# Performance work log

Hardware: AMD Instinct MI355X
Metric: run time of the kernel (lower is better)

## Reference

```python
import jax, jax.numpy as jnp
import numpy as np

NUM_CLASS = 31
B = 4096
F_IN = 2048
F_BOT = 256


def setup_inputs() -> dict:
    key = jax.random.key(0)
    ks = jax.random.split(key, 6)
    return {
        "source": jax.random.normal(ks[0], (B, F_IN), dtype=jnp.float32),
        "target": jax.random.normal(ks[1], (B, F_IN), dtype=jnp.float32),
        "W_b": jax.random.normal(ks[2], (F_IN, F_BOT), dtype=jnp.float32) * (1.0 / np.sqrt(F_IN)),
        "b_b": jnp.zeros((F_BOT,), dtype=jnp.float32),
        "W_c": jax.random.normal(ks[3], (F_BOT, NUM_CLASS), dtype=jnp.float32) * (1.0 / np.sqrt(F_BOT)),
        "b_c": jnp.zeros((NUM_CLASS,), dtype=jnp.float32),
        "source_label": jax.random.randint(ks[4], (B,), 0, NUM_CLASS, dtype=jnp.int64),
    }


def _conf_margin(logits, labels):
    # get_confidence_output_margin: softmax confidence margin vs best wrong class
    conf = jax.nn.softmax(logits, axis=-1)
    mask = jax.nn.one_hot(labels, NUM_CLASS, dtype=conf.dtype)
    targets_conf = jnp.sum(conf * mask, axis=1)
    max_excl_conf = jnp.max(conf * (1.0 - mask), axis=1)
    return targets_conf - max_excl_conf


def _pairwise_sqdist(s, t):
    # ||x_p - x_q||^2 computed as a single GEMM + broadcast (replaces python double loop)
    s2 = jnp.sum(s * s, axis=1)  # [Bs]
    t2 = jnp.sum(t * t, axis=1)  # [Bt]
    d2 = s2[:, None] + t2[None, :] - 2.0 * (s @ t.T)
    return jnp.maximum(d2, 0.0)


def reference(source, target, W_b, b_b, W_c, b_c, source_label):
    # bottleneck: Linear + ReLU (shared weights for both domains)
    src = jax.nn.relu(source @ W_b + b_b)  # [B, 256]
    tar = jax.nn.relu(target @ W_b + b_b)  # [B, 256]

    src_clf = src @ W_c + b_c  # [B, 31]
    tar_clf = tar @ W_c + b_c  # [B, 31]

    # cross entropy on source
    logp = jax.nn.log_softmax(src_clf, axis=-1)
    clf_loss = -jnp.mean(jnp.take_along_axis(logp, source_label[:, None], axis=1))

    src_margin = _conf_margin(src_clf, source_label)
    tar_margin = _conf_margin(tar_clf, jnp.argmax(tar_clf, axis=1))

    # no_grad diagnostics: MMD + Gaussian kernel means (amplitude=1, sigma in {1,5})
    delta = jnp.mean(src, axis=0) - jnp.mean(tar, axis=0)
    curr_mmd = jax.lax.stop_gradient(delta @ delta)
    d2 = _pairwise_sqdist(src, tar)  # [B, B]
    curr_gk1 = jax.lax.stop_gradient(jnp.mean(jnp.exp(-0.5 * d2)))
    curr_gk5 = jax.lax.stop_gradient(jnp.mean(jnp.exp(-d2 / 50.0)))

    return jnp.concatenate([
        jnp.stack([clf_loss, curr_mmd, curr_gk1, curr_gk5]),
        src_margin,
        tar_margin,
    ])  # [4 + 2B]
```

## Files before the change

### kernel.cpp

```cpp
#include <hip/hip_runtime.h>
#include <hip/hip_bf16.h>
#include <stdint.h>

#define DI __device__ __forceinline__

typedef float f32x4 __attribute__((ext_vector_type(4)));
typedef short bf16x8 __attribute__((ext_vector_type(8)));

DI uint16_t f2bf(float f) {
    union { float f; uint32_t u; } v; v.f = f;
    uint32_t r = v.u + 0x7FFF + ((v.u >> 16) & 1);
    return (uint16_t)(r >> 16);
}
DI float bf2f(uint16_t h) {
    union { uint32_t u; float f; } v; v.u = ((uint32_t)h) << 16;
    return v.f;
}
DI uint32_t pk_bf16(float x, float y) {
    __hip_bfloat162 h = __float22bfloat162_rn(make_float2(x, y));
    union { __hip_bfloat162 h; uint32_t u; } v; v.h = h; return v.u;
}
DI void gl_lds16(const void* g, void* l) {
    __builtin_amdgcn_global_load_lds(
        (__attribute__((address_space(1))) void*)(uintptr_t)g,
        (__attribute__((address_space(3))) void*)(uintptr_t)l,
        16, 0, 0);
}

__global__ void k_prep(const float* __restrict__ Wb, uint16_t* __restrict__ WbT,
                       const float* __restrict__ Wc, uint16_t* __restrict__ WcT) {
    if (blockIdx.x == 512) {
        int tid = threadIdx.x;
        for (int idx = tid; idx < 32 * 256; idx += 256) {
            int n = idx >> 8, k = idx & 255;
            WcT[idx] = (n < 31) ? f2bf(Wc[k * 31 + n]) : (uint16_t)0;
        }
        return;
    }
    __shared__ float t[32][33];
    int kb = blockIdx.x & 63, nb = blockIdx.x >> 6;
    int tx = threadIdx.x & 31, ty0 = (threadIdx.x >> 5) * 4;
    for (int i = 0; i < 4; ++i)
        t[ty0 + i][tx] = Wb[(kb * 32 + ty0 + i) * 256 + nb * 32 + tx];
    __syncthreads();
    for (int i = 0; i < 4; ++i)
        WbT[(nb * 32 + ty0 + i) * 2048 + kb * 32 + tx] = f2bf(t[tx][ty0 + i]);
}

__launch_bounds__(256, 4)
__global__ void k_bottleneck(const float* __restrict__ src, const float* __restrict__ tgt,
                             const uint16_t* __restrict__ WbT, const float* __restrict__ bbias,
                             uint16_t* __restrict__ Y) {
    __shared__ __align__(16) uint8_t lds[24576];
    int tid = threadIdx.x, lane = tid & 63, w = tid >> 6;
    int bm = blockIdx.x >> 2, bn = blockIdx.x & 3;
    int rowbase = bm * 32, n0 = bn * 64;
    const float* Xr = (rowbase < 4096) ? src + (size_t)rowbase * 2048
                                       : tgt + (size_t)(rowbase - 4096) * 2048;
    int rl = lane & 15, kq = lane >> 4;

    int as = tid >> 6;
    const float* Ag = Xr + (size_t)((as & 1) * 16 + rl) * 2048 + (as >> 1) * 32 + kq * 8;
    uint8_t* Aw0 = lds + tid * 16;
    uint8_t* Aw1 = lds + 4096 + tid * 16;

    const uint16_t* Bg[4];
    uint8_t* Bl[4];
    for (int i = 0; i < 4; ++i) {
        int sb = w * 4 + i, kb = sb >> 2, wseg = sb & 3;
        Bg[i] = WbT + (size_t)(n0 + wseg * 16 + rl) * 2048 + kb * 32 + kq * 8;
        Bl[i] = lds + 8192 + sb * 1024;
    }

    f32x4 acc[2] = {};
    for (int t = 0; t < 16; ++t) {
        if (t) __syncthreads();
        int k0 = t * 128;
        for (int i = 0; i < 4; ++i) gl_lds16(Bg[i] + k0, Bl[i]);
        float4 x0 = *(const float4*)(Ag + k0);
        float4 x1 = *(const float4*)(Ag + k0 + 4);
        float4 x2 = *(const float4*)(Ag + k0 + 64);
        float4 x3 = *(const float4*)(Ag + k0 + 68);
        uint4 u0, u1;
        u0.x = pk_bf16(x0.x, x0.y); u0.y = pk_bf16(x0.z, x0.w);
        u0.z = pk_bf16(x1.x, x1.y); u0.w = pk_bf16(x1.z, x1.w);
        u1.x = pk_bf16(x2.x, x2.y); u1.y = pk_bf16(x2.z, x2.w);
        u1.z = pk_bf16(x3.x, x3.y); u1.w = pk_bf16(x3.z, x3.w);
        *(uint4*)Aw0 = u0;
        *(uint4*)Aw1 = u1;
        __syncthreads();
#pragma unroll
        for (int kb = 0; kb < 4; ++kb) {
            bf16x8 a0 = *(const bf16x8*)(lds + kb * 2048 + lane * 16);
            bf16x8 a1 = *(const bf16x8*)(lds + kb * 2048 + 1024 + lane * 16);
            bf16x8 b  = *(const bf16x8*)(lds + 8192 + kb * 4096 + w * 1024 + lane * 16);
            acc[0] = __builtin_amdgcn_mfma_f32_16x16x32_bf16(a0, b, acc[0], 0, 0, 0);
            acc[1] = __builtin_amdgcn_mfma_f32_16x16x32_bf16(a1, b, acc[1], 0, 0, 0);
        }
    }
    int col = n0 + w * 16 + rl;
    float bias = bbias[col];
    for (int mi = 0; mi < 2; ++mi)
        for (int j = 0; j < 4; ++j) {
            int row = rowbase + mi * 16 + kq * 4 + j;
            float v = fmaxf(acc[mi][j] + bias, 0.f);
            Y[(size_t)row * 256 + col] = f2bf(v);
        }
}

__global__ void k_stats(const uint16_t* __restrict__ Y, float* __restrict__ s2t2,
                        float* __restrict__ part) {
    __shared__ float sred[4][256];
    int tid = threadIdx.x, cg = tid & 63, rs = tid >> 6;
    int r0 = blockIdx.x * 16;
    float a0 = 0.f, a1 = 0.f, a2 = 0.f, a3 = 0.f;
    for (int it = 0; it < 4; ++it) {
        int row = r0 + it * 4 + rs;
        ushort4 v = *(const ushort4*)(Y + (size_t)row * 256 + cg * 4);
        float f0 = bf2f(v.x), f1 = bf2f(v.y), f2 = bf2f(v.z), f3 = bf2f(v.w);
        a0 += f0; a1 += f1; a2 += f2; a3 += f3;
        float s = f0 * f0 + f1 * f1 + f2 * f2 + f3 * f3;
        for (int m = 1; m < 64; m <<= 1) s += __shfl_xor(s, m);
        if (cg == 0) s2t2[row] = s;
    }
    sred[rs][cg * 4 + 0] = a0; sred[rs][cg * 4 + 1] = a1;
    sred[rs][cg * 4 + 2] = a2; sred[rs][cg * 4 + 3] = a3;
    __syncthreads();
    if (rs == 0)
        for (int i = 0; i < 4; ++i) {
            int col = cg * 4 + i;
            part[blockIdx.x * 256 + col] =
                sred[0][col] + sred[1][col] + sred[2][col] + sred[3][col];
        }
}

__launch_bounds__(64)
__global__ void k_classifier(const uint16_t* __restrict__ Y, const uint16_t* __restrict__ WcT,
                             const float* __restrict__ bc, const int* __restrict__ labels,
                             float* __restrict__ out_margin, float* __restrict__ ce_part) {
    int lane = threadIdx.x;
    int r0 = blockIdx.x * 16;
    bool is_src = (r0 < 4096);
    int rl = lane & 15, kq = lane >> 4;
    const uint16_t* Ap = Y + (size_t)(r0 + rl) * 256 + kq * 8;
    const uint16_t* Bp = WcT + (size_t)rl * 256 + kq * 8;
    f32x4 acc[2] = {};
#pragma unroll
    for (int kb = 0; kb < 8; ++kb) {
        bf16x8 a  = *(const bf16x8*)(Ap + kb * 32);
        bf16x8 b0 = *(const bf16x8*)(Bp + kb * 32);
        bf16x8 b1 = *(const bf16x8*)(Bp + 16 * 256 + kb * 32);
        acc[0] = __builtin_amdgcn_mfma_f32_16x16x32_bf16(a, b0, acc[0], 0, 0, 0);
        acc[1] = __builtin_amdgcn_mfma_f32_16x16x32_bf16(a, b1, acc[1], 0, 0, 0);
    }
    int c0 = rl, c1 = 16 + rl;
    float bc0 = bc[c0];
    float bc1 = (c1 < 31) ? bc[c1] : 0.f;
    float ce_local = 0.f;
    for (int j = 0; j < 4; ++j) {
        int row = r0 + kq * 4 + j;
        float v0 = acc[0][j] + bc0;
        float v1 = (c1 < 31) ? (acc[1][j] + bc1) : -1e30f;
        float mx = fmaxf(v0, v1);
        for (int m = 1; m < 16; m <<= 1) mx = fmaxf(mx, __shfl_xor(mx, m, 16));
        float e0 = __expf(v0 - mx);
        float e1 = (c1 < 31) ? __expf(v1 - mx) : 0.f;
        float ssum = e0 + e1;
        for (int m = 1; m < 16; m <<= 1) ssum += __shfl_xor(ssum, m, 16);
        float inv = 1.f / ssum;
        float conf0 = e0 * inv, conf1 = e1 * inv;
        int lab;
        if (is_src) {
            lab = labels[row];
        } else {
            float bv; int bi;
            if (v0 >= v1) { bv = v0; bi = c0; } else { bv = v1; bi = c1; }
            for (int m = 1; m < 16; m <<= 1) {
                float ov = __shfl_xor(bv, m, 16);
                int oi = __shfl_xor(bi, m, 16);
                if (ov > bv || (ov == bv && oi < bi)) { bv = ov; bi = oi; }
            }
            lab = bi;
        }
        float tc = (c0 == lab ? conf0 : 0.f) + (c1 == lab ? conf1 : 0.f);
        for (int m = 1; m < 16; m <<= 1) tc += __shfl_xor(tc, m, 16);
        float ex = fmaxf(c0 == lab ? -1.f : conf0,
                         (c1 == lab || c1 >= 31) ? -1.f : conf1);
        for (int m = 1; m < 16; m <<= 1) ex = fmaxf(ex, __shfl_xor(ex, m, 16));
        if (c0 == 0) out_margin[row] = tc - ex;
        if (is_src) {
            float vl = (c0 == lab) ? v0 : ((c1 == lab) ? v1 : -1e30f);
            for (int m = 1; m < 16; m <<= 1) vl = fmaxf(vl, __shfl_xor(vl, m, 16));
            if (c0 == 0) ce_local += -(vl - mx - __logf(ssum));
        }
    }
    ce_local += __shfl_xor(ce_local, 16);
    ce_local += __shfl_xor(ce_local, 32);
    if (lane == 0) ce_part[blockIdx.x] = is_src ? ce_local : 0.f;
}

__launch_bounds__(256)
__global__ void k_pairwise(const uint16_t* __restrict__ Y, const float* __restrict__ s2t2,
                           float* __restrict__ gk_part) {
    __shared__ __align__(16) uint8_t lds[32768];
    int tid = threadIdx.x, lane = tid & 63, w = tid >> 6;
    int m0 = blockIdx.x * 128, n0 = blockIdx.y * 128;
    int cc = (lane >> 4) ^ (lane & 3) ^ ((lane >> 2) & 3);
    int wm = (w & 1) * 64, wn = (w >> 1) * 64;
    f32x4 acc[4][4] = {};
    for (int h = 0; h < 4; ++h) {
        if (h) __syncthreads();
        int k0 = h * 64;
        for (int i = 0; i < 4; ++i) {
            int s = w * 4 + i;
            int kb = s >> 3, r0 = (s & 7) * 16;
            int r = r0 + (lane >> 2), p = lane & 3;
            int c = p ^ (r & 3) ^ ((r >> 2) & 3);
            gl_lds16(Y + (size_t)(m0 + r) * 256 + k0 + kb * 32 + c * 8, lds + s * 1024);
            gl_lds16(Y + (size_t)(4096 + n0 + r) * 256 + k0 + kb * 32 + c * 8,
                     lds + 16384 + s * 1024);
        }
        __syncthreads();
        for (int kb = 0; kb < 2; ++kb) {
            bf16x8 a[4], b[4];
            for (int mi = 0; mi < 4; ++mi) {
                int r = wm + mi * 16 + (lane & 15);
                a[mi] = *(const bf16x8*)(lds + kb * 8192 + r * 64 + cc * 16);
            }
            for (int nf = 0; nf < 4; ++nf) {
                int rn = wn + nf * 16 + (lane & 15);
                b[nf] = *(const bf16x8*)(lds + 16384 + kb * 8192 + rn * 64 + cc * 16);
            }
            for (int mi = 0; mi < 4; ++mi)
                for (int nf = 0; nf < 4; ++nf)
                    acc[mi][nf] = __builtin_amdgcn_mfma_f32_16x16x32_bf16(
                        a[mi], b[nf], acc[mi][nf], 0, 0, 0);
        }
    }
    float t2v[4];
    for (int nf = 0; nf < 4; ++nf)
        t2v[nf] = s2t2[4096 + n0 + wn + nf * 16 + (lane & 15)];
    float g1 = 0.f, g5 = 0.f;
    for (int mi = 0; mi < 4; ++mi) {
        int rbase = m0 + wm + mi * 16 + (lane >> 4) * 4;
        float s2v[4];
        for (int j = 0; j < 4; ++j) s2v[j] = s2t2[rbase + j];
        for (int nf = 0; nf < 4; ++nf)
            for (int j = 0; j < 4; ++j) {
                float d2 = s2v[j] + t2v[nf] - 2.f * acc[mi][nf][j];
                d2 = fmaxf(d2, 0.f);
                g1 += __expf(-0.5f * d2);
                g5 += __expf(-0.02f * d2);
            }
    }
    for (int m = 1; m < 64; m <<= 1) { g1 += __shfl_xor(g1, m); g5 += __shfl_xor(g5, m); }
    __syncthreads();
    float* red = (float*)lds;
    if (lane == 0) { red[w * 2] = g1; red[w * 2 + 1] = g5; }
    __syncthreads();
    if (tid == 0) {
        int bid = blockIdx.y * 32 + blockIdx.x;
        gk_part[bid * 2]     = red[0] + red[2] + red[4] + red[6];
        gk_part[bid * 2 + 1] = red[1] + red[3] + red[5] + red[7];
    }
}

__global__ void k_finalize(const float* __restrict__ colsum_part,
                           const float* __restrict__ gk_part,
                           const float* __restrict__ ce_part, float* __restrict__ d_out) {
    __shared__ float red[4][4];
    int tid = threadIdx.x, lane = tid & 63, w = tid >> 6;
    float cs = 0.f, ct = 0.f;
    for (int b = 0; b < 256; ++b)   cs += colsum_part[b * 256 + tid];
    for (int b = 256; b < 512; ++b) ct += colsum_part[b * 256 + tid];
    float delta = (cs - ct) * (1.f / 4096.f);
    float sq = delta * delta;
    float g1 = 0.f, g5 = 0.f;
    for (int i = 0; i < 4; ++i) {
        int p = tid * 4 + i;
        g1 += gk_part[p * 2];
        g5 += gk_part[p * 2 + 1];
    }
    float ce = ce_part[tid] + ce_part[tid + 256];
    for (int m = 1; m < 64; m <<= 1) {
        sq += __shfl_xor(sq, m);
        g1 += __shfl_xor(g1, m);
        g5 += __shfl_xor(g5, m);
        ce += __shfl_xor(ce, m);
    }
    if (lane == 0) { red[w][0] = sq; red[w][1] = g1; red[w][2] = g5; red[w][3] = ce; }
    __syncthreads();
    if (tid == 0) {
        d_out[0] = (red[0][3] + red[1][3] + red[2][3] + red[3][3]) * (1.f / 4096.f);
        d_out[1] = red[0][0] + red[1][0] + red[2][0] + red[3][0];
        d_out[2] = (red[0][1] + red[1][1] + red[2][1] + red[3][1]) * 5.9604644775390625e-08f;
        d_out[3] = (red[0][2] + red[1][2] + red[2][2] + red[3][2]) * 5.9604644775390625e-08f;
    }
}

extern "C" void kernel_launch(void* const* d_in, const int* in_sizes, int n_in,
                              void* d_out, int out_size, void* d_ws, size_t ws_size,
                              hipStream_t stream) {
    const float* source = (const float*)d_in[0];
    const float* target = (const float*)d_in[1];
    const float* Wb     = (const float*)d_in[2];
    const float* bb     = (const float*)d_in[3];
    const float* Wc     = (const float*)d_in[4];
    const float* bc     = (const float*)d_in[5];
    const int*   labels = (const int*)d_in[6];
    float* out = (float*)d_out;
    uint8_t* ws = (uint8_t*)d_ws;

    uint16_t* Y    = (uint16_t*)(ws);
    uint16_t* WbT  = (uint16_t*)(ws + 4194304);
    uint16_t* WcT  = (uint16_t*)(ws + 5242880);
    float*    s2t2 = (float*)(ws + 5259264);
    float* colsum_part = (float*)(ws + 4194304);
    float* gk_part     = (float*)(ws + 4194304 + 524288);
    float* ce_part     = (float*)(ws + 4194304 + 532480);

    k_prep<<<513, 256, 0, stream>>>(Wb, WbT, Wc, WcT);
    k_bottleneck<<<1024, 256, 0, stream>>>(source, target, WbT, bb, Y);
    k_stats<<<512, 256, 0, stream>>>(Y, s2t2, colsum_part);
    k_classifier<<<512, 64, 0, stream>>>(Y, WcT, bc, labels, out + 4, ce_part);
    k_pairwise<<<dim3(32, 32), 256, 0, stream>>>(Y, s2t2, gk_part);
    k_finalize<<<1, 256, 0, stream>>>(colsum_part, gk_part, ce_part, out);
}
```

Before: 203.3 us.

## Double-buffer bottleneck GEMM with register-resident A and wider N tiles

```diff
diff --git a/kernel.cpp b/kernel.cpp
--- a/kernel.cpp
+++ b/kernel.cpp
@@ -47,64 +47,98 @@
         WbT[(nb * 32 + ty0 + i) * 2048 + kb * 32 + tx] = f2bf(t[tx][ty0 + i]);
 }
 
-__launch_bounds__(256, 4)
+__launch_bounds__(256, 2)
 __global__ void k_bottleneck(const float* __restrict__ src, const float* __restrict__ tgt,
                              const uint16_t* __restrict__ WbT, const float* __restrict__ bbias,
                              uint16_t* __restrict__ Y) {
-    __shared__ __align__(16) uint8_t lds[24576];
+    __shared__ __align__(16) uint8_t lds[32768];
     int tid = threadIdx.x, lane = tid & 63, w = tid >> 6;
-    int bm = blockIdx.x >> 2, bn = blockIdx.x & 3;
-    int rowbase = bm * 32, n0 = bn * 64;
+    int bm = blockIdx.x >> 1, bn = blockIdx.x & 1;
+    int rowbase = bm * 32, n0 = bn * 128;
     const float* Xr = (rowbase < 4096) ? src + (size_t)rowbase * 2048
                                        : tgt + (size_t)(rowbase - 4096) * 2048;
     int rl = lane & 15, kq = lane >> 4;
 
-    int as = tid >> 6;
-    const float* Ag = Xr + (size_t)((as & 1) * 16 + rl) * 2048 + (as >> 1) * 32 + kq * 8;
-    uint8_t* Aw0 = lds + tid * 16;
-    uint8_t* Aw1 = lds + 4096 + tid * 16;
+    const float* Ab = Xr + (size_t)rl * 2048 + kq * 8;
 
     const uint16_t* Bg[4];
     uint8_t* Bl[4];
     for (int i = 0; i < 4; ++i) {
-        int sb = w * 4 + i, kb = sb >> 2, wseg = sb & 3;
-        Bg[i] = WbT + (size_t)(n0 + wseg * 16 + rl) * 2048 + kb * 32 + kq * 8;
-        Bl[i] = lds + 8192 + sb * 1024;
-    }
-
-    f32x4 acc[2] = {};
-    for (int t = 0; t < 16; ++t) {
-        if (t) __syncthreads();
-        int k0 = t * 128;
-        for (int i = 0; i < 4; ++i) gl_lds16(Bg[i] + k0, Bl[i]);
-        float4 x0 = *(const float4*)(Ag + k0);
-        float4 x1 = *(const float4*)(Ag + k0 + 4);
-        float4 x2 = *(const float4*)(Ag + k0 + 64);
-        float4 x3 = *(const float4*)(Ag + k0 + 68);
-        uint4 u0, u1;
-        u0.x = pk_bf16(x0.x, x0.y); u0.y = pk_bf16(x0.z, x0.w);
-        u0.z = pk_bf16(x1.x, x1.y); u0.w = pk_bf16(x1.z, x1.w);
-        u1.x = pk_bf16(x2.x, x2.y); u1.y = pk_bf16(x2.z, x2.w);
-        u1.z = pk_bf16(x3.x, x3.y); u1.w = pk_bf16(x3.z, x3.w);
-        *(uint4*)Aw0 = u0;
-        *(uint4*)Aw1 = u1;
+        int s = w * 4 + i, kb = s >> 3, nf = s & 7;
+        Bg[i] = WbT + (size_t)(n0 + nf * 16 + rl) * 2048 + kb * 32 + kq * 8;
+        Bl[i] = lds + s * 1024;
+    }
+
+    f32x4 acc[2][2] = {};
+    float4 a0[2][2][2], a1[2][2][2];
+
+    for (int i = 0; i < 4; ++i) gl_lds16(Bg[i], Bl[i]);
+#pragma unroll
+    for (int mi = 0; mi < 2; ++mi)
+#pragma unroll
+        for (int kb = 0; kb < 2; ++kb) {
+            const float* p = Ab + (size_t)mi * 16 * 2048 + kb * 32;
+            a0[mi][kb][0] = *(const float4*)(p);
+            a0[mi][kb][1] = *(const float4*)(p + 4);
+        }
+    __syncthreads();
+
+#pragma unroll
+    for (int t = 0; t < 32; ++t) {
+        const int cur = t & 1;
+        if (t < 31) {
+            int k0n = (t + 1) * 64;
+#pragma unroll
+            for (int mi = 0; mi < 2; ++mi)
+#pragma unroll
+                for (int kb = 0; kb < 2; ++kb) {
+                    const float* p = Ab + (size_t)mi * 16 * 2048 + kb * 32 + k0n;
+                    if (cur == 0) {
+                        a1[mi][kb][0] = *(const float4*)(p);
+                        a1[mi][kb][1] = *(const float4*)(p + 4);
+                    } else {
+                        a0[mi][kb][0] = *(const float4*)(p);
+                        a0[mi][kb][1] = *(const float4*)(p + 4);
+                    }
+                }
+            for (int i = 0; i < 4; ++i)
+                gl_lds16(Bg[i] + k0n, Bl[i] + (cur ^ 1) * 16384);
+        }
+        union { uint4 u; bf16x8 v; } af[2][2];
+#pragma unroll
+        for (int mi = 0; mi < 2; ++mi)
+#pragma unroll
+            for (int kb = 0; kb < 2; ++kb) {
+                float4 x0 = (cur == 0) ? a0[mi][kb][0] : a1[mi][kb][0];
+                float4 x1 = (cur == 0) ? a0[mi][kb][1] : a1[mi][kb][1];
+                af[mi][kb].u.x = pk_bf16(x0.x, x0.y);
+                af[mi][kb].u.y = pk_bf16(x0.z, x0.w);
+                af[mi][kb].u.z = pk_bf16(x1.x, x1.y);
+                af[mi][kb].u.w = pk_bf16(x1.z, x1.w);
+            }
+#pragma unroll
+        for (int kb = 0; kb < 2; ++kb)
+#pragma unroll
+            for (int nfl = 0; nfl < 2; ++nfl) {
+                bf16x8 b = *(const bf16x8*)(lds + cur * 16384 +
+                                            (kb * 8 + w * 2 + nfl) * 1024 + lane * 16);
+                acc[0][nfl] = __builtin_amdgcn_mfma_f32_16x16x32_bf16(
+                    af[0][kb].v, b, acc[0][nfl], 0, 0, 0);
+                acc[1][nfl] = __builtin_amdgcn_mfma_f32_16x16x32_bf16(
+                    af[1][kb].v, b, acc[1][nfl], 0, 0, 0);
+            }
         __syncthreads();
-#pragma unroll
-        for (int kb = 0; kb < 4; ++kb) {
-            bf16x8 a0 = *(const bf16x8*)(lds + kb * 2048 + lane * 16);
-            bf16x8 a1 = *(const bf16x8*)(lds + kb * 2048 + 1024 + lane * 16);
-            bf16x8 b  = *(const bf16x8*)(lds + 8192 + kb * 4096 + w * 1024 + lane * 16);
-            acc[0] = __builtin_amdgcn_mfma_f32_16x16x32_bf16(a0, b, acc[0], 0, 0, 0);
-            acc[1] = __builtin_amdgcn_mfma_f32_16x16x32_bf16(a1, b, acc[1], 0, 0, 0);
-        }
-    }
-    int col = n0 + w * 16 + rl;
-    float bias = bbias[col];
+    }
+
     for (int mi = 0; mi < 2; ++mi)
-        for (int j = 0; j < 4; ++j) {
-            int row = rowbase + mi * 16 + kq * 4 + j;
-            float v = fmaxf(acc[mi][j] + bias, 0.f);
-            Y[(size_t)row * 256 + col] = f2bf(v);
+        for (int nfl = 0; nfl < 2; ++nfl) {
+            int col = n0 + w * 32 + nfl * 16 + rl;
+            float bias = bbias[col];
+            for (int j = 0; j < 4; ++j) {
+                int row = rowbase + mi * 16 + kq * 4 + j;
+                float v = fmaxf(acc[mi][nfl][j] + bias, 0.f);
+                Y[(size_t)row * 256 + col] = f2bf(v);
+            }
         }
 }
 
@@ -271,7 +305,9 @@
     __shared__ float red[4][4];
     int tid = threadIdx.x, lane = tid & 63, w = tid >> 6;
     float cs = 0.f, ct = 0.f;
+#pragma unroll 8
     for (int b = 0; b < 256; ++b)   cs += colsum_part[b * 256 + tid];
+#pragma unroll 8
     for (int b = 256; b < 512; ++b) ct += colsum_part[b * 256 + tid];
     float delta = (cs - ct) * (1.f / 4096.f);
     float sq = delta * delta;
@@ -320,7 +356,7 @@
     float* ce_part     = (float*)(ws + 4194304 + 532480);
 
     k_prep<<<513, 256, 0, stream>>>(Wb, WbT, Wc, WcT);
-    k_bottleneck<<<1024, 256, 0, stream>>>(source, target, WbT, bb, Y);
+    k_bottleneck<<<512, 256, 0, stream>>>(source, target, WbT, bb, Y);
     k_stats<<<512, 256, 0, stream>>>(Y, s2t2, colsum_part);
     k_classifier<<<512, 64, 0, stream>>>(Y, WcT, bc, labels, out + 4, ce_part);
     k_pairwise<<<dim3(32, 32), 256, 0, stream>>>(Y, s2t2, gk_part);
```

Measured after the change: 229.7 us. 13.0% more time.

## Store weights and bottleneck output in MFMA fragment layout, drop LDS in bottleneck GEMM

Applied to the files above, without the earlier changes.

```diff
diff --git a/kernel.cpp b/kernel.cpp
--- a/kernel.cpp
+++ b/kernel.cpp
@@ -27,129 +27,134 @@
         16, 0, 0);
 }
 
-__global__ void k_prep(const float* __restrict__ Wb, uint16_t* __restrict__ WbT,
-                       const float* __restrict__ Wc, uint16_t* __restrict__ WcT) {
-    if (blockIdx.x == 512) {
-        int tid = threadIdx.x;
-        for (int idx = tid; idx < 32 * 256; idx += 256) {
-            int n = idx >> 8, k = idx & 255;
-            WcT[idx] = (n < 31) ? f2bf(Wc[k * 31 + n]) : (uint16_t)0;
-        }
-        return;
-    }
-    __shared__ float t[32][33];
-    int kb = blockIdx.x & 63, nb = blockIdx.x >> 6;
-    int tx = threadIdx.x & 31, ty0 = (threadIdx.x >> 5) * 4;
-    for (int i = 0; i < 4; ++i)
-        t[ty0 + i][tx] = Wb[(kb * 32 + ty0 + i) * 256 + nb * 32 + tx];
-    __syncthreads();
-    for (int i = 0; i < 4; ++i)
-        WbT[(nb * 32 + ty0 + i) * 2048 + kb * 32 + tx] = f2bf(t[tx][ty0 + i]);
-}
-
-__launch_bounds__(256, 4)
+
+__global__ void k_prep(const float* __restrict__ Wb, uint16_t* __restrict__ Bf,
+                       const float* __restrict__ Wc, uint16_t* __restrict__ Wcf) {
+    __shared__ float wlds[8192];
+    int tid = threadIdx.x;
+    if (blockIdx.x < 64) {
+        int c = blockIdx.x;
+        for (int r = 0; r < 32; ++r)
+            wlds[r * 256 + tid] = Wb[(size_t)(c * 32 + r) * 256 + tid];
+        __syncthreads();
+        for (int e = tid; e < 1024; e += 256) {
+            int nf = e >> 6, ln = e & 63, erl = ln & 15, ekq = ln >> 4;
+            ushort o[8];
+            for (int i = 0; i < 8; ++i) {
+                int kl = (i < 4) ? (ekq * 4 + i) : (16 + ekq * 4 + (i - 4));
+                o[i] = f2bf(wlds[kl * 256 + nf * 16 + erl]);
+            }
+            *(uint4*)(Bf + ((size_t)c * 16 + nf) * 512 + ln * 8) = *(uint4*)o;
+        }
+    } else {
+        for (int idx = tid; idx < 256 * 31; idx += 256) wlds[idx] = Wc[idx];
+        __syncthreads();
+        for (int e = tid; e < 1024; e += 256) {
+            int kb = e >> 7, rest = e & 127, nf = rest >> 6, ln = rest & 63;
+            int erl = ln & 15, ekq = ln >> 4;
+            ushort o[8];
+            for (int i = 0; i < 8; ++i) {
+                int k = kb * 32 + ekq * 8 + i, n = nf * 16 + erl;
+                o[i] = (n < 31) ? f2bf(wlds[k * 31 + n]) : (ushort)0;
+            }
+            *(uint4*)(Wcf + ((size_t)(kb * 2 + nf)) * 512 + ln * 8) = *(uint4*)o;
+        }
+    }
+}
+
+__launch_bounds__(256, 1)
 __global__ void k_bottleneck(const float* __restrict__ src, const float* __restrict__ tgt,
-                             const uint16_t* __restrict__ WbT, const float* __restrict__ bbias,
-                             uint16_t* __restrict__ Y) {
-    __shared__ __align__(16) uint8_t lds[24576];
+                             const uint16_t* __restrict__ Bf, const float* __restrict__ bbias,
+                             uint16_t* __restrict__ Yf) {
     int tid = threadIdx.x, lane = tid & 63, w = tid >> 6;
     int bm = blockIdx.x >> 2, bn = blockIdx.x & 3;
-    int rowbase = bm * 32, n0 = bn * 64;
+    int rowbase = bm * 128 + w * 32;
     const float* Xr = (rowbase < 4096) ? src + (size_t)rowbase * 2048
                                        : tgt + (size_t)(rowbase - 4096) * 2048;
     int rl = lane & 15, kq = lane >> 4;
-
-    int as = tid >> 6;
-    const float* Ag = Xr + (size_t)((as & 1) * 16 + rl) * 2048 + (as >> 1) * 32 + kq * 8;
-    uint8_t* Aw0 = lds + tid * 16;
-    uint8_t* Aw1 = lds + 4096 + tid * 16;
-
-    const uint16_t* Bg[4];
-    uint8_t* Bl[4];
-    for (int i = 0; i < 4; ++i) {
-        int sb = w * 4 + i, kb = sb >> 2, wseg = sb & 3;
-        Bg[i] = WbT + (size_t)(n0 + wseg * 16 + rl) * 2048 + kb * 32 + kq * 8;
-        Bl[i] = lds + 8192 + sb * 1024;
-    }
-
-    f32x4 acc[2] = {};
-    for (int t = 0; t < 16; ++t) {
-        if (t) __syncthreads();
-        int k0 = t * 128;
-        for (int i = 0; i < 4; ++i) gl_lds16(Bg[i] + k0, Bl[i]);
-        float4 x0 = *(const float4*)(Ag + k0);
-        float4 x1 = *(const float4*)(Ag + k0 + 4);
-        float4 x2 = *(const float4*)(Ag + k0 + 64);
-        float4 x3 = *(const float4*)(Ag + k0 + 68);
-        uint4 u0, u1;
-        u0.x = pk_bf16(x0.x, x0.y); u0.y = pk_bf16(x0.z, x0.w);
-        u0.z = pk_bf16(x1.x, x1.y); u0.w = pk_bf16(x1.z, x1.w);
-        u1.x = pk_bf16(x2.x, x2.y); u1.y = pk_bf16(x2.z, x2.w);
-        u1.z = pk_bf16(x3.x, x3.y); u1.w = pk_bf16(x3.z, x3.w);
-        *(uint4*)Aw0 = u0;
-        *(uint4*)Aw1 = u1;
-        __syncthreads();
+    const float* A0 = Xr + (size_t)rl * 2048 + kq * 4;
+    const float* A1 = Xr + (size_t)(16 + rl) * 2048 + kq * 4;
+    const uint16_t* Bp = Bf + (size_t)(bn * 4) * 512 + lane * 8;
+
+    f32x4 acc[2][4] = {};
 #pragma unroll
-        for (int kb = 0; kb < 4; ++kb) {
-            bf16x8 a0 = *(const bf16x8*)(lds + kb * 2048 + lane * 16);
-            bf16x8 a1 = *(const bf16x8*)(lds + kb * 2048 + 1024 + lane * 16);
-            bf16x8 b  = *(const bf16x8*)(lds + 8192 + kb * 4096 + w * 1024 + lane * 16);
-            acc[0] = __builtin_amdgcn_mfma_f32_16x16x32_bf16(a0, b, acc[0], 0, 0, 0);
-            acc[1] = __builtin_amdgcn_mfma_f32_16x16x32_bf16(a1, b, acc[1], 0, 0, 0);
-        }
-    }
-    int col = n0 + w * 16 + rl;
-    float bias = bbias[col];
-    for (int mi = 0; mi < 2; ++mi)
-        for (int j = 0; j < 4; ++j) {
-            int row = rowbase + mi * 16 + kq * 4 + j;
-            float v = fmaxf(acc[mi][j] + bias, 0.f);
-            Y[(size_t)row * 256 + col] = f2bf(v);
-        }
-}
-
-__global__ void k_stats(const uint16_t* __restrict__ Y, float* __restrict__ s2t2,
+    for (int c = 0; c < 64; ++c) {
+        int k0 = c * 32;
+        float4 x00 = *(const float4*)(A0 + k0);
+        float4 x01 = *(const float4*)(A0 + k0 + 16);
+        float4 x10 = *(const float4*)(A1 + k0);
+        float4 x11 = *(const float4*)(A1 + k0 + 16);
+        bf16x8 b[4];
+#pragma unroll
+        for (int nf = 0; nf < 4; ++nf)
+            b[nf] = *(const bf16x8*)(Bp + ((size_t)c * 16 + nf) * 512);
+        union { uint4 u; bf16x8 v; } a0, a1;
+        a0.u.x = pk_bf16(x00.x, x00.y); a0.u.y = pk_bf16(x00.z, x00.w);
+        a0.u.z = pk_bf16(x01.x, x01.y); a0.u.w = pk_bf16(x01.z, x01.w);
+        a1.u.x = pk_bf16(x10.x, x10.y); a1.u.y = pk_bf16(x10.z, x10.w);
+        a1.u.z = pk_bf16(x11.x, x11.y); a1.u.w = pk_bf16(x11.z, x11.w);
+#pragma unroll
+        for (int nf = 0; nf < 4; ++nf) {
+            acc[0][nf] = __builtin_amdgcn_mfma_f32_16x16x32_bf16(a0.v, b[nf], acc[0][nf], 0, 0, 0);
+            acc[1][nf] = __builtin_amdgcn_mfma_f32_16x16x32_bf16(a1.v, b[nf], acc[1][nf], 0, 0, 0);
+        }
+    }
+    for (int nf = 0; nf < 4; ++nf) {
+        int col = bn * 64 + nf * 16 + rl;
+        float bias = bbias[col];
+        for (int mi = 0; mi < 2; ++mi) {
+            size_t fi = (size_t)((bm * 8 + w * 2 + mi) * 8 + bn * 2 + (nf >> 1));
+            for (int j = 0; j < 4; ++j) {
+                float v = fmaxf(acc[mi][nf][j] + bias, 0.f);
+                int ln = (kq * 4 + j) + ((nf & 1) * 2 + (rl >> 3)) * 16;
+                Yf[fi * 512 + ln * 8 + (rl & 7)] = f2bf(v);
+            }
+        }
+    }
+}
+
+__global__ void k_stats(const uint16_t* __restrict__ Yf, float* __restrict__ s2t2,
                         float* __restrict__ part) {
-    __shared__ float sred[4][256];
-    int tid = threadIdx.x, cg = tid & 63, rs = tid >> 6;
-    int r0 = blockIdx.x * 16;
-    float a0 = 0.f, a1 = 0.f, a2 = 0.f, a3 = 0.f;
-    for (int it = 0; it < 4; ++it) {
-        int row = r0 + it * 4 + rs;
-        ushort4 v = *(const ushort4*)(Y + (size_t)row * 256 + cg * 4);
-        float f0 = bf2f(v.x), f1 = bf2f(v.y), f2 = bf2f(v.z), f3 = bf2f(v.w);
-        a0 += f0; a1 += f1; a2 += f2; a3 += f3;
-        float s = f0 * f0 + f1 * f1 + f2 * f2 + f3 * f3;
-        for (int m = 1; m < 64; m <<= 1) s += __shfl_xor(s, m);
-        if (cg == 0) s2t2[row] = s;
-    }
-    sred[rs][cg * 4 + 0] = a0; sred[rs][cg * 4 + 1] = a1;
-    sred[rs][cg * 4 + 2] = a2; sred[rs][cg * 4 + 3] = a3;
+    __shared__ float rowred[8][16];
+    int tid = threadIdx.x, lane = tid & 63, w = tid >> 6;
+    int mb = blockIdx.x;
+    int rl = lane & 15, kq = lane >> 4;
+    for (int ci = 0; ci < 2; ++ci) {
+        int c = w * 2 + ci;
+        bf16x8 vv = *(const bf16x8*)(Yf + ((size_t)mb * 8 + c) * 512 + lane * 8);
+        union { bf16x8 v; ushort s[8]; } u; u.v = vv;
+        float f[8], s2 = 0.f;
+        for (int i = 0; i < 8; ++i) { f[i] = bf2f(u.s[i]); s2 += f[i] * f[i]; }
+        s2 += __shfl_xor(s2, 16); s2 += __shfl_xor(s2, 32);
+        if (kq == 0) rowred[c][rl] = s2;
+        for (int m = 1; m < 16; m <<= 1)
+            for (int i = 0; i < 8; ++i) f[i] += __shfl_xor(f[i], m);
+        if (rl == 0)
+            for (int i = 0; i < 8; ++i)
+                part[(size_t)mb * 256 + c * 32 + kq * 8 + i] = f[i];
+    }
     __syncthreads();
-    if (rs == 0)
-        for (int i = 0; i < 4; ++i) {
-            int col = cg * 4 + i;
-            part[blockIdx.x * 256 + col] =
-                sred[0][col] + sred[1][col] + sred[2][col] + sred[3][col];
-        }
+    if (tid < 16) {
+        float s = 0.f;
+        for (int c = 0; c < 8; ++c) s += rowred[c][tid];
+        s2t2[mb * 16 + tid] = s;
+    }
 }
 
 __launch_bounds__(64)
-__global__ void k_classifier(const uint16_t* __restrict__ Y, const uint16_t* __restrict__ WcT,
+__global__ void k_classifier(const uint16_t* __restrict__ Yf, const uint16_t* __restrict__ Wcf,
                              const float* __restrict__ bc, const int* __restrict__ labels,
                              float* __restrict__ out_margin, float* __restrict__ ce_part) {
     int lane = threadIdx.x;
-    int r0 = blockIdx.x * 16;
+    int mb = blockIdx.x, r0 = mb * 16;
     bool is_src = (r0 < 4096);
     int rl = lane & 15, kq = lane >> 4;
-    const uint16_t* Ap = Y + (size_t)(r0 + rl) * 256 + kq * 8;
-    const uint16_t* Bp = WcT + (size_t)rl * 256 + kq * 8;
     f32x4 acc[2] = {};
 #pragma unroll
     for (int kb = 0; kb < 8; ++kb) {
-        bf16x8 a  = *(const bf16x8*)(Ap + kb * 32);
-        bf16x8 b0 = *(const bf16x8*)(Bp + kb * 32);
-        bf16x8 b1 = *(const bf16x8*)(Bp + 16 * 256 + kb * 32);
+        bf16x8 a  = *(const bf16x8*)(Yf + ((size_t)mb * 8 + kb) * 512 + lane * 8);
+        bf16x8 b0 = *(const bf16x8*)(Wcf + ((size_t)(kb * 2 + 0)) * 512 + lane * 8);
+        bf16x8 b1 = *(const bf16x8*)(Wcf + ((size_t)(kb * 2 + 1)) * 512 + lane * 8);
         acc[0] = __builtin_amdgcn_mfma_f32_16x16x32_bf16(a, b0, acc[0], 0, 0, 0);
         acc[1] = __builtin_amdgcn_mfma_f32_16x16x32_bf16(a, b1, acc[1], 0, 0, 0);
     }
@@ -200,37 +205,31 @@
 }
 
 __launch_bounds__(256)
-__global__ void k_pairwise(const uint16_t* __restrict__ Y, const float* __restrict__ s2t2,
+__global__ void k_pairwise(const uint16_t* __restrict__ Yf, const float* __restrict__ s2t2,
                            float* __restrict__ gk_part) {
     __shared__ __align__(16) uint8_t lds[32768];
     int tid = threadIdx.x, lane = tid & 63, w = tid >> 6;
     int m0 = blockIdx.x * 128, n0 = blockIdx.y * 128;
-    int cc = (lane >> 4) ^ (lane & 3) ^ ((lane >> 2) & 3);
     int wm = (w & 1) * 64, wn = (w >> 1) * 64;
     f32x4 acc[4][4] = {};
     for (int h = 0; h < 4; ++h) {
         if (h) __syncthreads();
-        int k0 = h * 64;
-        for (int i = 0; i < 4; ++i) {
-            int s = w * 4 + i;
-            int kb = s >> 3, r0 = (s & 7) * 16;
-            int r = r0 + (lane >> 2), p = lane & 3;
-            int c = p ^ (r & 3) ^ ((r >> 2) & 3);
-            gl_lds16(Y + (size_t)(m0 + r) * 256 + k0 + kb * 32 + c * 8, lds + s * 1024);
-            gl_lds16(Y + (size_t)(4096 + n0 + r) * 256 + k0 + kb * 32 + c * 8,
-                     lds + 16384 + s * 1024);
+        for (int i = 0; i < 8; ++i) {
+            int s = w * 8 + i;
+            int t = s & 15, mbi = t >> 1, ci = t & 1;
+            size_t fi = (s < 16)
+                ? ((size_t)(m0 / 16 + mbi) * 8 + 2 * h + ci)
+                : ((size_t)(256 + n0 / 16 + mbi) * 8 + 2 * h + ci);
+            gl_lds16(Yf + fi * 512 + lane * 8,
+                     lds + ((s < 16) ? 0 : 16384) + t * 1024 + lane * 16);
         }
         __syncthreads();
         for (int kb = 0; kb < 2; ++kb) {
             bf16x8 a[4], b[4];
-            for (int mi = 0; mi < 4; ++mi) {
-                int r = wm + mi * 16 + (lane & 15);
-                a[mi] = *(const bf16x8*)(lds + kb * 8192 + r * 64 + cc * 16);
-            }
-            for (int nf = 0; nf < 4; ++nf) {
-                int rn = wn + nf * 16 + (lane & 15);
-                b[nf] = *(const bf16x8*)(lds + 16384 + kb * 8192 + rn * 64 + cc * 16);
-            }
+            for (int mi = 0; mi < 4; ++mi)
+                a[mi] = *(const bf16x8*)(lds + (((w & 1) * 4 + mi) * 2 + kb) * 1024 + lane * 16);
+            for (int nf = 0; nf < 4; ++nf)
+                b[nf] = *(const bf16x8*)(lds + 16384 + (((w >> 1) * 4 + nf) * 2 + kb) * 1024 + lane * 16);
             for (int mi = 0; mi < 4; ++mi)
                 for (int nf = 0; nf < 4; ++nf)
                     acc[mi][nf] = __builtin_amdgcn_mfma_f32_16x16x32_bf16(
@@ -271,8 +270,10 @@
     __shared__ float red[4][4];
     int tid = threadIdx.x, lane = tid & 63, w = tid >> 6;
     float cs = 0.f, ct = 0.f;
-    for (int b = 0; b < 256; ++b)   cs += colsum_part[b * 256 + tid];
-    for (int b = 256; b < 512; ++b) ct += colsum_part[b * 256 + tid];
+#pragma unroll 8
+    for (int b = 0; b < 256; ++b)   cs += colsum_part[(size_t)b * 256 + tid];
+#pragma unroll 8
+    for (int b = 256; b < 512; ++b) ct += colsum_part[(size_t)b * 256 + tid];
     float delta = (cs - ct) * (1.f / 4096.f);
     float sq = delta * delta;
     float g1 = 0.f, g5 = 0.f;
@@ -311,18 +312,18 @@
     float* out = (float*)d_out;
     uint8_t* ws = (uint8_t*)d_ws;
 
-    uint16_t* Y    = (uint16_t*)(ws);
-    uint16_t* WbT  = (uint16_t*)(ws + 4194304);
-    uint16_t* WcT  = (uint16_t*)(ws + 5242880);
+    uint16_t* Yf   = (uint16_t*)(ws);
+    uint16_t* Bf   = (uint16_t*)(ws + 4194304);
+    uint16_t* Wcf  = (uint16_t*)(ws + 5242880);
     float*    s2t2 = (float*)(ws + 5259264);
     float* colsum_part = (float*)(ws + 4194304);
     float* gk_part     = (float*)(ws + 4194304 + 524288);
     float* ce_part     = (float*)(ws + 4194304 + 532480);
 
-    k_prep<<<513, 256, 0, stream>>>(Wb, WbT, Wc, WcT);
-    k_bottleneck<<<1024, 256, 0, stream>>>(source, target, WbT, bb, Y);
-    k_stats<<<512, 256, 0, stream>>>(Y, s2t2, colsum_part);
-    k_classifier<<<512, 64, 0, stream>>>(Y, WcT, bc, labels, out + 4, ce_part);
-    k_pairwise<<<dim3(32, 32), 256, 0, stream>>>(Y, s2t2, gk_part);
+    k_prep<<<65, 256, 0, stream>>>(Wb, Bf, Wc, Wcf);
+    k_bottleneck<<<256, 256, 0, stream>>>(source, target, Bf, bb, Yf);
+    k_stats<<<512, 256, 0, stream>>>(Yf, s2t2, colsum_part);
+    k_classifier<<<512, 64, 0, stream>>>(Yf, Wcf, bc, labels, out + 4, ce_part);
+    k_pairwise<<<dim3(32, 32), 256, 0, stream>>>(Yf, s2t2, gk_part);
     k_finalize<<<1, 256, 0, stream>>>(colsum_part, gk_part, ce_part, out);
 }
```

Result: slower. 216.3 us (+6.4%).
